# Kernel tuning notes

Hardware: AMD Instinct MI355X
Metric: run time of the kernel (lower is better)

The kernel has to match this reference:

```python
import jax, jax.numpy as jnp
import numpy as np

N_HEADS = 32
N_KV_HEADS = 8
HEAD_DIM = 128
DIM = 4096
WINDOW = 4096
BATCH = 32
START_POS = 4095


def setup_inputs() -> dict:
    key = jax.random.key(0)
    ks = jax.random.split(key, 6)
    s = 0.02
    return {
        "x": jax.random.normal(ks[0], (1, 1, BATCH, DIM), jnp.float32),
        "wqkv": jax.random.normal(ks[1], (DIM, (N_HEADS + 2 * N_KV_HEADS) * HEAD_DIM), jnp.float32) * s,
        "wo": jax.random.normal(ks[2], (DIM, DIM), jnp.float32) * s,
        "rot_mat": jax.random.normal(ks[3], (HEAD_DIM, HEAD_DIM), jnp.float32) * s,
        "cache_k": jax.random.normal(ks[4], (N_KV_HEADS, BATCH, WINDOW, HEAD_DIM), jnp.float32),
        "cache_v": jax.random.normal(ks[5], (N_KV_HEADS, BATCH, WINDOW, HEAD_DIM), jnp.float32),
        "start_pos": START_POS,
    }


def reference(x, wqkv, wo, rot_mat, cache_k, cache_v, start_pos):
    B = x.shape[2]
    D = HEAD_DIM
    group = N_HEADS // N_KV_HEADS  # 4 q heads per kv head (GQA)

    # fused QKV projection for the single decode token: [B, (nq+2*nkv)*D]
    xqkv = jnp.einsum('bh,hf->bf', x[0, 0], wqkv)
    q = xqkv[:, : N_HEADS * D].reshape(B, N_HEADS, D)
    k = xqkv[:, N_HEADS * D: (N_HEADS + N_KV_HEADS) * D].reshape(B, N_KV_HEADS, D)
    v = xqkv[:, (N_HEADS + N_KV_HEADS) * D:].reshape(B, N_KV_HEADS, D)

    # rotary embedding applied as a matmul by a [D, D] rotation matrix
    q = jnp.einsum('bnd,de->bne', q, rot_mat) * (D ** -0.5)
    k = jnp.einsum('bnd,de->bne', k, rot_mat)

    # sliding-window KV cache update at current_pos (cache: [nkv, B, W, D])
    current_pos = start_pos % WINDOW
    cache_k = cache_k.at[:, :, current_pos, :].set(jnp.transpose(k, (1, 0, 2)))
    cache_v = cache_v.at[:, :, current_pos, :].set(jnp.transpose(v, (1, 0, 2)))

    layer_slice = min(start_pos + 1, WINDOW)  # static python int
    keys = cache_k[:, :, :layer_slice]    # [nkv, B, S, D]
    values = cache_v[:, :, :layer_slice]  # [nkv, B, S, D]

    qg = q.reshape(B, N_KV_HEADS, group, D)
    scores = jnp.einsum('bkgd,kbsd->bkgs', qg, keys)       # [B, nkv, g, S]
    attn = jax.nn.softmax(scores, axis=-1)
    out = jnp.einsum('bkgs,kbsd->bkgd', attn, values)      # [B, nkv, g, D]
    out = out.reshape(B, N_HEADS * D)

    dense = out @ wo  # wo pre-transposed: [H, H], output features last
    return dense.reshape(1, 1, B, DIM)
```

## Files before the change

kernel.cpp:

```cpp
#include <hip/hip_runtime.h>
#include <math.h>

#define B 32
#define NH 32
#define NKV 8
#define GRP 4
#define HD 128
#define DIM 4096
#define NQKV 6144
#define WIN 4096
#define KS 32
#define SPLIT 16
#define SCHUNK (WIN / SPLIT)

__device__ __forceinline__ float fast_exp2(float x) {
#if __has_builtin(__builtin_amdgcn_exp2f)
  return __builtin_amdgcn_exp2f(x);
#else
  return exp2f(x);
#endif
}

__global__ __launch_bounds__(256)
void gemv32_partial(const float* __restrict__ X, const float* __restrict__ W,
                    float* __restrict__ part, int K, int N) {
  const int f  = blockIdx.x * 256 + threadIdx.x;
  const int kc = blockIdx.y;
  const int kchunk = K / KS;
  const int k0 = kc * kchunk;

  __shared__ float xs[128][36];

  float acc[B];
#pragma unroll
  for (int b = 0; b < B; ++b) acc[b] = 0.f;

  for (int kb = 0; kb < kchunk; kb += 128) {
    __syncthreads();
    for (int idx = threadIdx.x; idx < B * 128; idx += 256) {
      int bb = idx >> 7;
      int kk = idx & 127;
      xs[kk][bb] = X[(size_t)bb * K + (k0 + kb + kk)];
    }
    __syncthreads();

    const float* wp = W + (size_t)(k0 + kb) * N + f;
#pragma unroll 4
    for (int kk = 0; kk < 128; ++kk) {
      float w = wp[(size_t)kk * N];
      const float4* xr = (const float4*)&xs[kk][0];
#pragma unroll
      for (int b4 = 0; b4 < 8; ++b4) {
        float4 xv = xr[b4];
        acc[b4 * 4 + 0] += xv.x * w;
        acc[b4 * 4 + 1] += xv.y * w;
        acc[b4 * 4 + 2] += xv.z * w;
        acc[b4 * 4 + 3] += xv.w * w;
      }
    }
  }

  float* pp = part + (size_t)kc * B * N + f;
#pragma unroll
  for (int b = 0; b < B; ++b) pp[(size_t)b * N] = acc[b];
}

__global__ __launch_bounds__(256)
void reduce_partials(const float* __restrict__ part, float* __restrict__ out,
                     int total) {
  int idx = blockIdx.x * 256 + threadIdx.x;
  if (idx >= total) return;
  float s = 0.f;
#pragma unroll
  for (int kc = 0; kc < KS; ++kc) s += part[(size_t)kc * total + idx];
  out[idx] = s;
}

__global__ __launch_bounds__(128)
void rotary_kernel(const float* __restrict__ xqkv, const float* __restrict__ rot,
                   float* __restrict__ qrot, float* __restrict__ krot) {
  const int b = blockIdx.x;
  const int h = blockIdx.y;
  const int e = threadIdx.x;

  __shared__ float vec[HD];
  vec[e] = xqkv[(size_t)b * NQKV + h * HD + e];
  __syncthreads();

  float s = 0.f;
#pragma unroll 8
  for (int d = 0; d < HD; ++d) s += vec[d] * rot[d * HD + e];

  const float QSCALE = 0.08838834764831845f * 1.4426950408889634f;
  if (h < NH) {
    qrot[((size_t)b * NH + h) * HD + e] = s * QSCALE;
  } else {
    krot[((size_t)b * NKV + (h - NH)) * HD + e] = s;
  }
}

__global__ __launch_bounds__(256)
void attn_partial(const float* __restrict__ cache_k, const float* __restrict__ cache_v,
                  const float* __restrict__ qrot, const float* __restrict__ krot,
                  const float* __restrict__ xqkv, const int* __restrict__ start_pos,
                  float* __restrict__ o_part, float* __restrict__ l_part) {
  const int pair = blockIdx.x;
  const int b    = pair >> 3;
  const int kvh  = pair & 7;
  const int chunk = blockIdx.y;

  const int sp    = start_pos[0];
  const int cur   = sp & (WIN - 1);
  const int slice = (sp + 1 < WIN) ? (sp + 1) : WIN;

  const int tid  = threadIdx.x;
  const int wave = tid >> 6;
  const int lane = tid & 63;
  const int half = lane >> 5;
  const int l32  = lane & 31;
  const int hw   = wave * 2 + half;

  float4 q[GRP];
#pragma unroll
  for (int g = 0; g < GRP; ++g)
    q[g] = *(const float4*)(qrot + ((size_t)(b * NH + kvh * GRP + g)) * HD + l32 * 4);

  const float4* kbase = (const float4*)(cache_k + ((size_t)(kvh * B + b)) * WIN * HD);
  const float4* vbase = (const float4*)(cache_v + ((size_t)(kvh * B + b)) * WIN * HD);

  float  l[GRP] = {0.f, 0.f, 0.f, 0.f};
  float4 acc[GRP] = {};

  const int s0 = chunk * SCHUNK;
  int rem = slice - s0 - hw;
  int n_i = rem <= 0 ? 0 : ((rem + 7) >> 3);
  if (n_i > SCHUNK / 8) n_i = SCHUNK / 8;

  auto body = [&](float4 k4, float4 v4) {
    float s[GRP];
#pragma unroll
    for (int g = 0; g < GRP; ++g)
      s[g] = q[g].x * k4.x + q[g].y * k4.y + q[g].z * k4.z + q[g].w * k4.w;
#pragma unroll
    for (int off = 16; off > 0; off >>= 1) {
#pragma unroll
      for (int g = 0; g < GRP; ++g) s[g] += __shfl_xor(s[g], off);
    }
#pragma unroll
    for (int g = 0; g < GRP; ++g) {
      float w = fast_exp2(s[g]);
      l[g] += w;
      acc[g].x += w * v4.x; acc[g].y += w * v4.y;
      acc[g].z += w * v4.z; acc[g].w += w * v4.w;
    }
  };

  if (n_i > 0) {
    size_t rb = ((size_t)(s0 + hw)) * 32 + l32;
    float4 k4 = kbase[rb];
    float4 v4 = vbase[rb];
#pragma unroll 2
    for (int i = 1; i < n_i; ++i) {
      rb += 8 * 32;
      float4 kn = kbase[rb];
      float4 vn = vbase[rb];
      body(k4, v4);
      k4 = kn; v4 = vn;
    }
    body(k4, v4);
  }

  if (chunk == (cur >> 8) && hw == (cur & 7)) {
    float4 kst = kbase[(size_t)cur * 32 + l32];
    float4 vst = vbase[(size_t)cur * 32 + l32];
    const float4 knew = *(const float4*)(krot + ((size_t)(b * NKV + kvh)) * HD + l32 * 4);
    const float4 vnew = *(const float4*)(xqkv + (size_t)b * NQKV + (NH + NKV + kvh) * HD + l32 * 4);
    float sst[GRP], snw[GRP];
#pragma unroll
    for (int g = 0; g < GRP; ++g) {
      sst[g] = q[g].x * kst.x + q[g].y * kst.y + q[g].z * kst.z + q[g].w * kst.w;
      snw[g] = q[g].x * knew.x + q[g].y * knew.y + q[g].z * knew.z + q[g].w * knew.w;
    }
#pragma unroll
    for (int off = 16; off > 0; off >>= 1) {
#pragma unroll
      for (int g = 0; g < GRP; ++g) {
        sst[g] += __shfl_xor(sst[g], off);
        snw[g] += __shfl_xor(snw[g], off);
      }
    }
#pragma unroll
    for (int g = 0; g < GRP; ++g) {
      float wst = fast_exp2(sst[g]);
      float wnw = fast_exp2(snw[g]);
      l[g] += wnw - wst;
      acc[g].x += wnw * vnew.x - wst * vst.x;
      acc[g].y += wnw * vnew.y - wst * vst.y;
      acc[g].z += wnw * vnew.z - wst * vst.z;
      acc[g].w += wnw * vnew.w - wst * vst.w;
    }
  }

#pragma unroll
  for (int g = 0; g < GRP; ++g) {
    l[g] += __shfl_xor(l[g], 32);
    acc[g].x += __shfl_xor(acc[g].x, 32);
    acc[g].y += __shfl_xor(acc[g].y, 32);
    acc[g].z += __shfl_xor(acc[g].z, 32);
    acc[g].w += __shfl_xor(acc[g].w, 32);
  }

  __shared__ float red_l[4][GRP];
  __shared__ float red_o[4][GRP][HD];
  if (lane == 0) {
#pragma unroll
    for (int g = 0; g < GRP; ++g) red_l[wave][g] = l[g];
  }
  if (half == 0) {
#pragma unroll
    for (int g = 0; g < GRP; ++g)
      *(float4*)&red_o[wave][g][l32 * 4] = acc[g];
  }
  __syncthreads();

  const size_t pc = (size_t)pair * SPLIT + chunk;
  for (int idx = tid; idx < GRP * HD; idx += 256) {
    int g = idx >> 7, d = idx & 127;
    float o = red_o[0][g][d] + red_o[1][g][d] + red_o[2][g][d] + red_o[3][g][d];
    o_part[(pc * GRP + g) * HD + d] = o;
  }
  if (tid < GRP) {
    l_part[pc * GRP + tid] =
        red_l[0][tid] + red_l[1][tid] + red_l[2][tid] + red_l[3][tid];
  }
}

__global__ __launch_bounds__(128)
void attn_combine(const float* __restrict__ o_part, const float* __restrict__ l_part,
                  float* __restrict__ attn_out) {
  const int bid = blockIdx.x;
  const int b = bid >> 5, n = bid & 31;
  const int pair = b * NKV + (n >> 2);
  const int g = n & 3;
  const int d = threadIdx.x;

  float lsum = 0.f, osum = 0.f;
#pragma unroll
  for (int c = 0; c < SPLIT; ++c) {
    size_t pc = (size_t)pair * SPLIT + c;
    lsum += l_part[pc * GRP + g];
    osum += o_part[(pc * GRP + g) * HD + d];
  }
  attn_out[(size_t)b * DIM + n * HD + d] = osum / lsum;
}

extern "C" void kernel_launch(void* const* d_in, const int* in_sizes, int n_in,
                              void* d_out, int out_size, void* d_ws, size_t ws_size,
                              hipStream_t stream) {
  (void)in_sizes; (void)n_in; (void)out_size; (void)ws_size;

  const float* x    = (const float*)d_in[0];
  const float* wqkv = (const float*)d_in[1];
  const float* wo   = (const float*)d_in[2];
  const float* rot  = (const float*)d_in[3];
  const float* ck   = (const float*)d_in[4];
  const float* cv   = (const float*)d_in[5];
  const int*   sp   = (const int*)d_in[6];
  float* out = (float*)d_out;

  float* ws       = (float*)d_ws;
  float* part     = ws;
  float* o_part   = ws;
  float* xqkv     = part + (size_t)KS * B * NQKV;
  float* qrot     = xqkv + (size_t)B * NQKV;
  float* krot     = qrot + (size_t)B * NH * HD;
  float* l_part   = krot + (size_t)B * NKV * HD;
  float* attn_out = l_part + (size_t)B * NKV * SPLIT * GRP;

  gemv32_partial<<<dim3(NQKV / 256, KS), 256, 0, stream>>>(x, wqkv, part, DIM, NQKV);
  reduce_partials<<<(B * NQKV) / 256, 256, 0, stream>>>(part, xqkv, B * NQKV);

  rotary_kernel<<<dim3(B, NH + NKV), 128, 0, stream>>>(xqkv, rot, qrot, krot);

  attn_partial<<<dim3(B * NKV, SPLIT), 256, 0, stream>>>(ck, cv, qrot, krot, xqkv,
                                                         sp, o_part, l_part);
  attn_combine<<<B * NH, 128, 0, stream>>>(o_part, l_part, attn_out);

  gemv32_partial<<<dim3(DIM / 256, KS), 256, 0, stream>>>(attn_out, wo, part, DIM, DIM);
  reduce_partials<<<(B * DIM) / 256, 256, 0, stream>>>(part, out, B * DIM);
}
```

Before: 317.6 us.

## Process 16 rows per block iteration with 16 lanes per row in attention

Changes the attention partial kernel so each 64-lane wave covers four KV positions at once, with 16 lanes per position each loading two float4s (8 dims), instead of two positions per wave at 32 lanes each. This halves the shuffle-reduction depth per score and doubles the bytes each lane has in flight per iteration. The data-dependent trip count is replaced by a fixed WITER loop with a per-row predicate on the exp weight. The cost is more registers per thread for the duplicated q and accumulator halves, and loads for positions beyond the slice still happen.

```diff
diff --git a/kernel.cpp b/kernel.cpp
--- a/kernel.cpp
+++ b/kernel.cpp
@@ -12,6 +12,7 @@
 #define KS 32
 #define SPLIT 16
 #define SCHUNK (WIN / SPLIT)
+#define WITER (SCHUNK / 16)
 
 __device__ __forceinline__ float fast_exp2(float x) {
 #if __has_builtin(__builtin_amdgcn_exp2f)
@@ -116,110 +117,128 @@
   const int tid  = threadIdx.x;
   const int wave = tid >> 6;
   const int lane = tid & 63;
-  const int half = lane >> 5;
-  const int l32  = lane & 31;
-  const int hw   = wave * 2 + half;
-
-  float4 q[GRP];
-#pragma unroll
-  for (int g = 0; g < GRP; ++g)
-    q[g] = *(const float4*)(qrot + ((size_t)(b * NH + kvh * GRP + g)) * HD + l32 * 4);
+  const int grp  = (lane >> 4) & 3;
+  const int s    = lane & 15;
+
+  float4 qa[GRP], qb[GRP];
+  {
+    const float* qbase = qrot + ((size_t)(b * NH + kvh * GRP)) * HD + s * 8;
+#pragma unroll
+    for (int h = 0; h < GRP; ++h) {
+      qa[h] = *(const float4*)(qbase + h * HD);
+      qb[h] = *(const float4*)(qbase + h * HD + 4);
+    }
+  }
 
   const float4* kbase = (const float4*)(cache_k + ((size_t)(kvh * B + b)) * WIN * HD);
   const float4* vbase = (const float4*)(cache_v + ((size_t)(kvh * B + b)) * WIN * HD);
 
   float  l[GRP] = {0.f, 0.f, 0.f, 0.f};
-  float4 acc[GRP] = {};
-
-  const int s0 = chunk * SCHUNK;
-  int rem = slice - s0 - hw;
-  int n_i = rem <= 0 ? 0 : ((rem + 7) >> 3);
-  if (n_i > SCHUNK / 8) n_i = SCHUNK / 8;
-
-  auto body = [&](float4 k4, float4 v4) {
-    float s[GRP];
-#pragma unroll
-    for (int g = 0; g < GRP; ++g)
-      s[g] = q[g].x * k4.x + q[g].y * k4.y + q[g].z * k4.z + q[g].w * k4.w;
-#pragma unroll
-    for (int off = 16; off > 0; off >>= 1) {
-#pragma unroll
-      for (int g = 0; g < GRP; ++g) s[g] += __shfl_xor(s[g], off);
-    }
-#pragma unroll
-    for (int g = 0; g < GRP; ++g) {
-      float w = fast_exp2(s[g]);
-      l[g] += w;
-      acc[g].x += w * v4.x; acc[g].y += w * v4.y;
-      acc[g].z += w * v4.z; acc[g].w += w * v4.w;
-    }
-  };
-
-  if (n_i > 0) {
-    size_t rb = ((size_t)(s0 + hw)) * 32 + l32;
-    float4 k4 = kbase[rb];
-    float4 v4 = vbase[rb];
+  float4 aa[GRP] = {}, ab[GRP] = {};
+
+  const int s0  = chunk * SCHUNK;
+  const int off = wave * 4 + grp;
+
+#define ATTN_BODY9(KA, KB, VA, VB, P)                                        \
+  {                                                                          \
+    float t[GRP];                                                            \
+    _Pragma("unroll")                                                        \
+    for (int h = 0; h < GRP; ++h)                                            \
+      t[h] = qa[h].x*KA.x + qa[h].y*KA.y + qa[h].z*KA.z + qa[h].w*KA.w       \
+           + qb[h].x*KB.x + qb[h].y*KB.y + qb[h].z*KB.z + qb[h].w*KB.w;      \
+    _Pragma("unroll")                                                        \
+    for (int off2 = 1; off2 <= 8; off2 <<= 1) {                              \
+      _Pragma("unroll")                                                      \
+      for (int h = 0; h < GRP; ++h) t[h] += __shfl_xor(t[h], off2);          \
+    }                                                                        \
+    const bool ok = (P) < slice;                                             \
+    _Pragma("unroll")                                                        \
+    for (int h = 0; h < GRP; ++h) {                                          \
+      float w = ok ? fast_exp2(t[h]) : 0.f;                                  \
+      l[h] += w;                                                             \
+      aa[h].x += w*VA.x; aa[h].y += w*VA.y; aa[h].z += w*VA.z; aa[h].w += w*VA.w; \
+      ab[h].x += w*VB.x; ab[h].y += w*VB.y; ab[h].z += w*VB.z; ab[h].w += w*VB.w; \
+    }                                                                        \
+  }
+
+  {
+    int p = s0 + off;
+    size_t fi = (size_t)p * 32 + s * 2;
+    float4 kA = kbase[fi], kB = kbase[fi + 1];
+    float4 vA = vbase[fi], vB = vbase[fi + 1];
 #pragma unroll 2
-    for (int i = 1; i < n_i; ++i) {
-      rb += 8 * 32;
-      float4 kn = kbase[rb];
-      float4 vn = vbase[rb];
-      body(k4, v4);
-      k4 = kn; v4 = vn;
-    }
-    body(k4, v4);
-  }
-
-  if (chunk == (cur >> 8) && hw == (cur & 7)) {
-    float4 kst = kbase[(size_t)cur * 32 + l32];
-    float4 vst = vbase[(size_t)cur * 32 + l32];
-    const float4 knew = *(const float4*)(krot + ((size_t)(b * NKV + kvh)) * HD + l32 * 4);
-    const float4 vnew = *(const float4*)(xqkv + (size_t)b * NQKV + (NH + NKV + kvh) * HD + l32 * 4);
-    float sst[GRP], snw[GRP];
-#pragma unroll
-    for (int g = 0; g < GRP; ++g) {
-      sst[g] = q[g].x * kst.x + q[g].y * kst.y + q[g].z * kst.z + q[g].w * kst.w;
-      snw[g] = q[g].x * knew.x + q[g].y * knew.y + q[g].z * knew.z + q[g].w * knew.w;
-    }
-#pragma unroll
-    for (int off = 16; off > 0; off >>= 1) {
-#pragma unroll
-      for (int g = 0; g < GRP; ++g) {
-        sst[g] += __shfl_xor(sst[g], off);
-        snw[g] += __shfl_xor(snw[g], off);
+    for (int i = 1; i < WITER; ++i) {
+      fi += 16 * 32;
+      float4 kA2 = kbase[fi], kB2 = kbase[fi + 1];
+      float4 vA2 = vbase[fi], vB2 = vbase[fi + 1];
+      ATTN_BODY9(kA, kB, vA, vB, p);
+      kA = kA2; kB = kB2; vA = vA2; vB = vB2;
+      p += 16;
+    }
+    ATTN_BODY9(kA, kB, vA, vB, p);
+  }
+
+  if (chunk == (cur >> 8) && off == (cur & 15)) {
+    size_t fi = (size_t)cur * 32 + s * 2;
+    float4 ksA = kbase[fi], ksB = kbase[fi + 1];
+    float4 vsA = vbase[fi], vsB = vbase[fi + 1];
+    const float* kp = krot + ((size_t)(b * NKV + kvh)) * HD + s * 8;
+    const float* vp = xqkv + (size_t)b * NQKV + (NH + NKV + kvh) * HD + s * 8;
+    float4 knA = *(const float4*)kp,       knB = *(const float4*)(kp + 4);
+    float4 vnA = *(const float4*)vp,       vnB = *(const float4*)(vp + 4);
+
+    float tst[GRP], tnw[GRP];
+#pragma unroll
+    for (int h = 0; h < GRP; ++h) {
+      tst[h] = qa[h].x*ksA.x + qa[h].y*ksA.y + qa[h].z*ksA.z + qa[h].w*ksA.w
+             + qb[h].x*ksB.x + qb[h].y*ksB.y + qb[h].z*ksB.z + qb[h].w*ksB.w;
+      tnw[h] = qa[h].x*knA.x + qa[h].y*knA.y + qa[h].z*knA.z + qa[h].w*knA.w
+             + qb[h].x*knB.x + qb[h].y*knB.y + qb[h].z*knB.z + qb[h].w*knB.w;
+    }
+#pragma unroll
+    for (int off2 = 1; off2 <= 8; off2 <<= 1) {
+#pragma unroll
+      for (int h = 0; h < GRP; ++h) {
+        tst[h] += __shfl_xor(tst[h], off2);
+        tnw[h] += __shfl_xor(tnw[h], off2);
       }
     }
 #pragma unroll
-    for (int g = 0; g < GRP; ++g) {
-      float wst = fast_exp2(sst[g]);
-      float wnw = fast_exp2(snw[g]);
-      l[g] += wnw - wst;
-      acc[g].x += wnw * vnew.x - wst * vst.x;
-      acc[g].y += wnw * vnew.y - wst * vst.y;
-      acc[g].z += wnw * vnew.z - wst * vst.z;
-      acc[g].w += wnw * vnew.w - wst * vst.w;
-    }
-  }
-
-#pragma unroll
-  for (int g = 0; g < GRP; ++g) {
-    l[g] += __shfl_xor(l[g], 32);
-    acc[g].x += __shfl_xor(acc[g].x, 32);
-    acc[g].y += __shfl_xor(acc[g].y, 32);
-    acc[g].z += __shfl_xor(acc[g].z, 32);
-    acc[g].w += __shfl_xor(acc[g].w, 32);
+    for (int h = 0; h < GRP; ++h) {
+      float wst = fast_exp2(tst[h]);
+      float wnw = fast_exp2(tnw[h]);
+      l[h] += wnw - wst;
+      aa[h].x += wnw*vnA.x - wst*vsA.x;  aa[h].y += wnw*vnA.y - wst*vsA.y;
+      aa[h].z += wnw*vnA.z - wst*vsA.z;  aa[h].w += wnw*vnA.w - wst*vsA.w;
+      ab[h].x += wnw*vnB.x - wst*vsB.x;  ab[h].y += wnw*vnB.y - wst*vsB.y;
+      ab[h].z += wnw*vnB.z - wst*vsB.z;  ab[h].w += wnw*vnB.w - wst*vsB.w;
+    }
+  }
+
+#pragma unroll
+  for (int lv = 16; lv <= 32; lv <<= 1) {
+#pragma unroll
+    for (int h = 0; h < GRP; ++h) {
+      l[h] += __shfl_xor(l[h], lv);
+      aa[h].x += __shfl_xor(aa[h].x, lv); aa[h].y += __shfl_xor(aa[h].y, lv);
+      aa[h].z += __shfl_xor(aa[h].z, lv); aa[h].w += __shfl_xor(aa[h].w, lv);
+      ab[h].x += __shfl_xor(ab[h].x, lv); ab[h].y += __shfl_xor(ab[h].y, lv);
+      ab[h].z += __shfl_xor(ab[h].z, lv); ab[h].w += __shfl_xor(ab[h].w, lv);
+    }
   }
 
   __shared__ float red_l[4][GRP];
   __shared__ float red_o[4][GRP][HD];
-  if (lane == 0) {
-#pragma unroll
-    for (int g = 0; g < GRP; ++g) red_l[wave][g] = l[g];
-  }
-  if (half == 0) {
-#pragma unroll
-    for (int g = 0; g < GRP; ++g)
-      *(float4*)&red_o[wave][g][l32 * 4] = acc[g];
+  if (lane < 16) {
+#pragma unroll
+    for (int h = 0; h < GRP; ++h) {
+      *(float4*)&red_o[wave][h][lane * 8]     = aa[h];
+      *(float4*)&red_o[wave][h][lane * 8 + 4] = ab[h];
+    }
+    if (lane == 0) {
+#pragma unroll
+      for (int h = 0; h < GRP; ++h) red_l[wave][h] = l[h];
+    }
   }
   __syncthreads();
 
```

New measurement: 360.6 us. 13.6% more time.

## Batch four KV rows per wave-half with double-buffered super-iteration loads

Applied to the files above, without the earlier changes.

The attention partial kernel now has each wave own an 8-row group inside each 32-row super-block. Every lane-half issues four K and four V float4 loads per iteration and prefetches the next super-block while computing the current one. Rows past the slice are masked instead of trimming the trip count. Launch bounds request 4 blocks per SM to cap registers. The goal is more memory-level parallelism on the bandwidth-bound cache stream, at the cost of higher register pressure and possible spills.

```diff
diff --git a/kernel.cpp b/kernel.cpp
--- a/kernel.cpp
+++ b/kernel.cpp
@@ -12,6 +12,7 @@
 #define KS 32
 #define SPLIT 16
 #define SCHUNK (WIN / SPLIT)
+#define NSUP (SCHUNK / 32)
 
 __device__ __forceinline__ float fast_exp2(float x) {
 #if __has_builtin(__builtin_amdgcn_exp2f)
@@ -99,7 +100,7 @@
   }
 }
 
-__global__ __launch_bounds__(256)
+__global__ __launch_bounds__(256, 4)
 void attn_partial(const float* __restrict__ cache_k, const float* __restrict__ cache_v,
                   const float* __restrict__ qrot, const float* __restrict__ krot,
                   const float* __restrict__ xqkv, const int* __restrict__ start_pos,
@@ -118,7 +119,6 @@
   const int lane = tid & 63;
   const int half = lane >> 5;
   const int l32  = lane & 31;
-  const int hw   = wave * 2 + half;
 
   float4 q[GRP];
 #pragma unroll
@@ -132,57 +132,72 @@
   float4 acc[GRP] = {};
 
   const int s0 = chunk * SCHUNK;
-  int rem = slice - s0 - hw;
-  int n_i = rem <= 0 ? 0 : ((rem + 7) >> 3);
-  if (n_i > SCHUNK / 8) n_i = SCHUNK / 8;
-
-  auto body = [&](float4 k4, float4 v4) {
-    float s[GRP];
-#pragma unroll
-    for (int g = 0; g < GRP; ++g)
-      s[g] = q[g].x * k4.x + q[g].y * k4.y + q[g].z * k4.z + q[g].w * k4.w;
-#pragma unroll
-    for (int off = 16; off > 0; off >>= 1) {
-#pragma unroll
-      for (int g = 0; g < GRP; ++g) s[g] += __shfl_xor(s[g], off);
-    }
-#pragma unroll
-    for (int g = 0; g < GRP; ++g) {
-      float w = fast_exp2(s[g]);
-      l[g] += w;
-      acc[g].x += w * v4.x; acc[g].y += w * v4.y;
-      acc[g].z += w * v4.z; acc[g].w += w * v4.w;
-    }
-  };
-
-  if (n_i > 0) {
-    size_t rb = ((size_t)(s0 + hw)) * 32 + l32;
-    float4 k4 = kbase[rb];
-    float4 v4 = vbase[rb];
-#pragma unroll 2
-    for (int i = 1; i < n_i; ++i) {
-      rb += 8 * 32;
-      float4 kn = kbase[rb];
-      float4 vn = vbase[rb];
-      body(k4, v4);
-      k4 = kn; v4 = vn;
-    }
-    body(k4, v4);
-  }
-
-  if (chunk == (cur >> 8) && hw == (cur & 7)) {
-    float4 kst = kbase[(size_t)cur * 32 + l32];
-    float4 vst = vbase[(size_t)cur * 32 + l32];
+
+#define SUPER_COMPUTE(KARR, VARR, PBASE)                                     \
+  {                                                                          \
+    _Pragma("unroll")                                                        \
+    for (int j = 0; j < 4; ++j) {                                            \
+      const int p = (PBASE) + 2 * j + half;                                  \
+      float s[GRP];                                                          \
+      _Pragma("unroll")                                                      \
+      for (int g = 0; g < GRP; ++g)                                          \
+        s[g] = q[g].x*KARR[j].x + q[g].y*KARR[j].y                           \
+             + q[g].z*KARR[j].z + q[g].w*KARR[j].w;                          \
+      _Pragma("unroll")                                                      \
+      for (int off = 1; off <= 16; off <<= 1) {                              \
+        _Pragma("unroll")                                                    \
+        for (int g = 0; g < GRP; ++g) s[g] += __shfl_xor(s[g], off);         \
+      }                                                                      \
+      const bool ok = p < slice;                                             \
+      _Pragma("unroll")                                                      \
+      for (int g = 0; g < GRP; ++g) {                                        \
+        float w = ok ? fast_exp2(s[g]) : 0.f;                                \
+        l[g] += w;                                                           \
+        acc[g].x += w * VARR[j].x; acc[g].y += w * VARR[j].y;                \
+        acc[g].z += w * VARR[j].z; acc[g].w += w * VARR[j].w;                \
+      }                                                                      \
+    }                                                                        \
+  }
+
+  {
+    float4 k[4], v[4], kn[4], vn[4];
+    size_t base = (size_t)(s0 + wave * 8 + half) * 32 + l32;
+#pragma unroll
+    for (int j = 0; j < 4; ++j) k[j] = kbase[base + (size_t)j * 64];
+#pragma unroll
+    for (int j = 0; j < 4; ++j) v[j] = vbase[base + (size_t)j * 64];
+
+    int pbase = s0 + wave * 8;
+#pragma unroll 1
+    for (int i = 1; i < NSUP; ++i) {
+      base += 32 * 32;
+#pragma unroll
+      for (int j = 0; j < 4; ++j) kn[j] = kbase[base + (size_t)j * 64];
+#pragma unroll
+      for (int j = 0; j < 4; ++j) vn[j] = vbase[base + (size_t)j * 64];
+
+      SUPER_COMPUTE(k, v, pbase);
+
+#pragma unroll
+      for (int j = 0; j < 4; ++j) { k[j] = kn[j]; v[j] = vn[j]; }
+      pbase += 32;
+    }
+    SUPER_COMPUTE(k, v, pbase);
+  }
+
+  if (chunk == (cur >> 8) && wave == ((cur >> 3) & 3) && half == (cur & 1)) {
+    const float4 kst = kbase[(size_t)cur * 32 + l32];
+    const float4 vst = vbase[(size_t)cur * 32 + l32];
     const float4 knew = *(const float4*)(krot + ((size_t)(b * NKV + kvh)) * HD + l32 * 4);
     const float4 vnew = *(const float4*)(xqkv + (size_t)b * NQKV + (NH + NKV + kvh) * HD + l32 * 4);
     float sst[GRP], snw[GRP];
 #pragma unroll
     for (int g = 0; g < GRP; ++g) {
-      sst[g] = q[g].x * kst.x + q[g].y * kst.y + q[g].z * kst.z + q[g].w * kst.w;
-      snw[g] = q[g].x * knew.x + q[g].y * knew.y + q[g].z * knew.z + q[g].w * knew.w;
-    }
-#pragma unroll
-    for (int off = 16; off > 0; off >>= 1) {
+      sst[g] = q[g].x*kst.x + q[g].y*kst.y + q[g].z*kst.z + q[g].w*kst.w;
+      snw[g] = q[g].x*knew.x + q[g].y*knew.y + q[g].z*knew.z + q[g].w*knew.w;
+    }
+#pragma unroll
+    for (int off = 1; off <= 16; off <<= 1) {
 #pragma unroll
       for (int g = 0; g < GRP; ++g) {
         sst[g] += __shfl_xor(sst[g], off);
@@ -194,10 +209,10 @@
       float wst = fast_exp2(sst[g]);
       float wnw = fast_exp2(snw[g]);
       l[g] += wnw - wst;
-      acc[g].x += wnw * vnew.x - wst * vst.x;
-      acc[g].y += wnw * vnew.y - wst * vst.y;
-      acc[g].z += wnw * vnew.z - wst * vst.z;
-      acc[g].w += wnw * vnew.w - wst * vst.w;
+      acc[g].x += wnw*vnew.x - wst*vst.x;
+      acc[g].y += wnw*vnew.y - wst*vst.y;
+      acc[g].z += wnw*vnew.z - wst*vst.z;
+      acc[g].w += wnw*vnew.w - wst*vst.w;
     }
   }
 
```

Measured after the change: 313.8 us. About the same (-1.2%).
